# Performance work log

Measured on AMD Instinct MI355X. Metric: run time of the kernel, lower is better.

## Reference

```python
import jax, jax.numpy as jnp
import numpy as np

B, N, D, H = 4, 2048, 1024, 64

def setup_inputs() -> dict:
    key = jax.random.key(0)
    ks = jax.random.split(key, 7)
    s = D ** -0.5  # torch Linear default init scale ~ U(-1/sqrt(fan_in), ...); scale randn similarly
    return {
        "x":  jax.random.normal(ks[0], (B, N, D), dtype=jnp.float32),
        "Wq": jax.random.normal(ks[1], (D, H), dtype=jnp.float32) * s,
        "bq": jax.random.normal(ks[2], (H,), dtype=jnp.float32) * s,
        "Wk": jax.random.normal(ks[3], (D, H), dtype=jnp.float32) * s,
        "bk": jax.random.normal(ks[4], (H,), dtype=jnp.float32) * s,
        "Wv": jax.random.normal(ks[5], (D, H), dtype=jnp.float32) * s,
        "bv": jax.random.normal(ks[6], (H,), dtype=jnp.float32) * s,
    }

def reference(x, Wq, bq, Wk, bk, Wv, bv):
    head_size = Wq.shape[1]
    q = x @ Wq + bq          # [B, N, H]
    k = x @ Wk + bk          # [B, N, H]
    v = x @ Wv + bv          # [B, N, H]
    scores = jnp.einsum("bid,bjd->bij", q, k)        # [B, N, N]
    # faithful to torch: keep upper triangle (col >= row), then mask exact zeros to -inf
    scores = jnp.triu(scores)
    scores = jnp.where(scores == 0, -jnp.inf, scores)
    attn = jax.nn.softmax(scores * (head_size ** -0.5), axis=-1)  # [B, N, N]
    # out = (V^T @ attn)^T  ==  attn^T @ V
    out = jnp.einsum("bji,bjh->bih", attn, v)         # [B, N, H]
    return out
```

## Files before the change

kernel.cpp:

```cpp
#include <hip/hip_runtime.h>
#include <math.h>

constexpr int kN = 2048;
constexpr int kD = 1024;

typedef __attribute__((ext_vector_type(8))) short bf16x8;
typedef __attribute__((ext_vector_type(4))) short bf16x4;
typedef __attribute__((ext_vector_type(4))) float f32x4;

#define MFMA(a, b, c) __builtin_amdgcn_mfma_f32_16x16x32_bf16(a, b, c, 0, 0, 0)

__device__ __forceinline__ short f2bf(float f) {
    unsigned u = __float_as_uint(f);
    u += 0x7fff + ((u >> 16) & 1);
    return (short)(u >> 16);
}

__device__ __forceinline__ void g2l(void* lds, const void* g, int nbytes, int t) {
    int lane = t & 63, w = t >> 6;
    for (int base = w * 1024; base < nbytes; base += 4096) {
        if (base + lane * 16 < nbytes) {
            __builtin_amdgcn_global_load_lds(
                (const __attribute__((address_space(1))) void*)((const char*)g + base + lane * 16),
                (__attribute__((address_space(3))) void*)((char*)lds + base),
                16, 0, 0);
        }
    }
}

__global__ __launch_bounds__(256) void prep_kernel(
        const float* __restrict__ Wq, const float* __restrict__ Wk,
        const float* __restrict__ Wv, const float* __restrict__ bq,
        const float* __restrict__ bk, const float* __restrict__ bv,
        short* __restrict__ Wt, float* __restrict__ bcat)
{
    int tid = blockIdx.x * 256 + threadIdx.x;
    int stride = gridDim.x * 256;
    for (int e = tid; e < 16 * 192 * 72; e += stride) {
        int kc = e / (192 * 72);
        int rem = e - kc * (192 * 72);
        int n = rem / 72, c = rem - n * 72;
        short v = 0;
        if (c < 64) {
            int d = kc * 64 + c;
            float wv = (n < 64) ? Wq[d * 64 + n]
                     : (n < 128) ? Wk[d * 64 + (n - 64)]
                     : Wv[d * 64 + (n - 128)];
            v = f2bf(wv);
        }
        Wt[e] = v;
    }
    if (tid < 192)
        bcat[tid] = (tid < 64) ? bq[tid] : (tid < 128) ? bk[tid - 64] : bv[tid - 128];
}

__global__ __launch_bounds__(256) void qkv_kernel(
        const float* __restrict__ x, const short* __restrict__ Wt,
        const float* __restrict__ bcat,
        short* __restrict__ gq, short* __restrict__ gk, short* __restrict__ vt)
{
    __shared__ __align__(16) short xs[2][16 * 72];
    __shared__ __align__(16) short wsm[2][192 * 72];
    const int t = threadIdx.x;
    const int w = t >> 6, lane = t & 63, l15 = lane & 15, q8 = lane >> 4;
    const int m0 = blockIdx.x * 16;
    const int xrow = t >> 4, xc4 = t & 15;
    const float* xbase = x + (size_t)(m0 + xrow) * kD + xc4 * 4;

    f32x4 acc[3];
    #pragma unroll
    for (int ct = 0; ct < 3; ++ct) acc[ct] = (f32x4){0.f, 0.f, 0.f, 0.f};

    float4 xcur = *(const float4*)(xbase + 0 * 64);
    g2l(wsm[0], Wt, 192 * 144, t);
    {
        bf16x4 pk = {f2bf(xcur.x), f2bf(xcur.y), f2bf(xcur.z), f2bf(xcur.w)};
        *(bf16x4*)&xs[0][xrow * 72 + xc4 * 4] = pk;
    }
    float4 xnxt = *(const float4*)(xbase + 1 * 64);
    __syncthreads();

    for (int kc = 0; kc < 16; ++kc) {
        const int cur = kc & 1, nb = cur ^ 1;
        if (kc < 15)
            g2l(wsm[nb], Wt + (size_t)(kc + 1) * 192 * 72, 192 * 144, t);

        bf16x8 a0 = *(const bf16x8*)&xs[cur][l15 * 72 + q8 * 8];
        bf16x8 a1 = *(const bf16x8*)&xs[cur][l15 * 72 + 32 + q8 * 8];
        #pragma unroll
        for (int ct = 0; ct < 3; ++ct) {
            int brow = w * 48 + ct * 16 + l15;
            bf16x8 b0 = *(const bf16x8*)&wsm[cur][brow * 72 + q8 * 8];
            bf16x8 b1 = *(const bf16x8*)&wsm[cur][brow * 72 + 32 + q8 * 8];
            acc[ct] = MFMA(a0, b0, acc[ct]);
            acc[ct] = MFMA(a1, b1, acc[ct]);
        }
        if (kc < 15) {
            bf16x4 pk = {f2bf(xnxt.x), f2bf(xnxt.y), f2bf(xnxt.z), f2bf(xnxt.w)};
            *(bf16x4*)&xs[nb][xrow * 72 + xc4 * 4] = pk;
            if (kc < 14)
                xnxt = *(const float4*)(xbase + (kc + 2) * 64);
        }
        __syncthreads();
    }

    const int bz = m0 >> 11;
    const int jt = (m0 & 2047) >> 6;
    const int jb = m0 & 63;
    #pragma unroll
    for (int ct = 0; ct < 3; ++ct) {
        int nb2 = w * 48 + ct * 16;
        int n = nb2 + l15;
        float bias = bcat[n];
        if (nb2 < 64) {
            #pragma unroll
            for (int r = 0; r < 4; ++r)
                gq[(size_t)(m0 + q8 * 4 + r) * 72 + n] = f2bf(acc[ct][r] + bias);
        } else if (nb2 < 128) {
            #pragma unroll
            for (int r = 0; r < 4; ++r)
                gk[(size_t)(m0 + q8 * 4 + r) * 72 + (n - 64)] = f2bf(acc[ct][r] + bias);
        } else {
            int h = n - 128;
            bf16x4 pk = {f2bf(acc[ct][0] + bias), f2bf(acc[ct][1] + bias),
                         f2bf(acc[ct][2] + bias), f2bf(acc[ct][3] + bias)};
            *(bf16x4*)&vt[((size_t)((bz * 32 + jt) * 64 + h)) * 72 + jb + q8 * 4] = pk;
        }
    }
}

__global__ __launch_bounds__(256) void stats_kernel(
        const short* __restrict__ gq, const short* __restrict__ gk,
        float* __restrict__ l2)
{
    __shared__ __align__(16) short qsm[64 * 72];
    __shared__ __align__(16) short ksm[2][64 * 72];
    const int t = threadIdx.x;
    const int w = t >> 6, lane = t & 63, l15 = lane & 15, q8 = lane >> 4;
    const int b = blockIdx.x;
    const int ic = b & 3, bz = (b >> 2) & 3, jt = b >> 4;
    const int j0 = jt * 64;
    const int ilo = ic * 512, ihi = ilo + 512;
    const int istart = (j0 > ilo) ? j0 : ilo;
    const int count = (istart < ihi) ? ((ihi - istart) >> 6) : 0;

    float lloc[4] = {0.f, 0.f, 0.f, 0.f};

    if (count > 0) {
        g2l(qsm, gq + (size_t)(bz * kN + j0) * 72, 64 * 144, t);
        g2l(ksm[0], gk + (size_t)(bz * kN + istart) * 72, 64 * 144, t);
        __syncthreads();
        int jrow = 16 * w + l15;
        bf16x8 a0 = *(const bf16x8*)&qsm[jrow * 72 + q8 * 8];
        bf16x8 a1 = *(const bf16x8*)&qsm[jrow * 72 + 32 + q8 * 8];

        for (int idx = 0; idx < count; ++idx) {
            const int cur = idx & 1;
            if (idx + 1 < count)
                g2l(ksm[cur ^ 1],
                    gk + (size_t)(bz * kN + istart + (idx + 1) * 64) * 72, 64 * 144, t);
            const int i0 = istart + idx * 64;
            #pragma unroll
            for (int it = 0; it < 4; ++it) {
                int irow = it * 16 + l15;
                bf16x8 b0 = *(const bf16x8*)&ksm[cur][irow * 72 + q8 * 8];
                bf16x8 b1 = *(const bf16x8*)&ksm[cur][irow * 72 + 32 + q8 * 8];
                f32x4 s = (f32x4){0.f, 0.f, 0.f, 0.f};
                s = MFMA(a0, b0, s);
                s = MFMA(a1, b1, s);
                int ig = i0 + it * 16 + l15;
                #pragma unroll
                for (int r = 0; r < 4; ++r) {
                    int jg = j0 + 16 * w + q8 * 4 + r;
                    float sv = s[r];
                    float e = __expf(sv * 0.125f);
                    lloc[r] += ((ig >= jg) && (sv != 0.0f)) ? e : 0.0f;
                }
            }
            __syncthreads();
        }
    }
    #pragma unroll
    for (int off = 1; off < 16; off <<= 1)
        #pragma unroll
        for (int r = 0; r < 4; ++r)
            lloc[r] += __shfl_xor(lloc[r], off);
    if (l15 == 0) {
        #pragma unroll
        for (int r = 0; r < 4; ++r)
            l2[ic * 8192 + bz * kN + j0 + 16 * w + q8 * 4 + r] = lloc[r];
    }
}

__global__ __launch_bounds__(256) void out_kernel(
        const short* __restrict__ gq, const short* __restrict__ gk,
        const short* __restrict__ vt, const float* __restrict__ l2,
        float* __restrict__ part)
{
    __shared__ __align__(16) short ksm[64 * 72];
    __shared__ __align__(16) short qsm[2][64 * 72];
    __shared__ __align__(16) short vsm[2][64 * 72];
    __shared__ __align__(16) short psm[64 * 72];
    __shared__ float rsm[2][64];
    const int t = threadIdx.x;
    const int w = t >> 6, lane = t & 63, l15 = lane & 15, q8 = lane >> 4;
    const int b = blockIdx.x;
    const int jc = b & 3, bz = (b >> 2) & 3, it = b >> 4;
    const int i0 = it * 64;
    const int jlo = jc * 512;
    const int jhi = (jlo + 512 < i0 + 64) ? (jlo + 512) : (i0 + 64);
    const int count = (jlo < jhi) ? ((jhi - jlo) >> 6) : 0;

    f32x4 oacc[4];
    #pragma unroll
    for (int i = 0; i < 4; ++i) oacc[i] = (f32x4){0.f, 0.f, 0.f, 0.f};

    if (count > 0) {
        g2l(ksm, gk + (size_t)(bz * kN + i0) * 72, 64 * 144, t);
        g2l(qsm[0], gq + (size_t)(bz * kN + jlo) * 72, 64 * 144, t);
        g2l(vsm[0], vt + (size_t)((bz * 32 + (jlo >> 6)) * 64) * 72, 64 * 144, t);
        if (t < 64) {
            int j = bz * kN + jlo + t;
            float l = l2[j] + l2[8192 + j] + l2[16384 + j] + l2[24576 + j];
            rsm[0][t] = (l > 0.f) ? 1.0f / l : 0.0f;
        }
        __syncthreads();

        for (int idx = 0; idx < count; ++idx) {
            const int cur = idx & 1, nb = cur ^ 1;
            const int j0s = jlo + idx * 64;
            if (idx + 1 < count) {
                g2l(qsm[nb], gq + (size_t)(bz * kN + j0s + 64) * 72, 64 * 144, t);
                g2l(vsm[nb], vt + (size_t)((bz * 32 + ((j0s + 64) >> 6)) * 64) * 72,
                    64 * 144, t);
                if (t < 64) {
                    int j = bz * kN + j0s + 64 + t;
                    float l = l2[j] + l2[8192 + j] + l2[16384 + j] + l2[24576 + j];
                    rsm[nb][t] = (l > 0.f) ? 1.0f / l : 0.0f;
                }
            }
            int jrow = 16 * w + l15;
            bf16x8 a0 = *(const bf16x8*)&qsm[cur][jrow * 72 + q8 * 8];
            bf16x8 a1 = *(const bf16x8*)&qsm[cur][jrow * 72 + 32 + q8 * 8];
            #pragma unroll
            for (int itile = 0; itile < 4; ++itile) {
                int irow = itile * 16 + l15;
                bf16x8 b0 = *(const bf16x8*)&ksm[irow * 72 + q8 * 8];
                bf16x8 b1 = *(const bf16x8*)&ksm[irow * 72 + 32 + q8 * 8];
                f32x4 s = (f32x4){0.f, 0.f, 0.f, 0.f};
                s = MFMA(a0, b0, s);
                s = MFMA(a1, b1, s);
                int ig = i0 + itile * 16 + l15;
                bf16x4 pk;
                #pragma unroll
                for (int r = 0; r < 4; ++r) {
                    int jl = 16 * w + q8 * 4 + r;
                    int jg = j0s + jl;
                    float sv = s[r];
                    float p = ((ig >= jg) && (sv != 0.0f))
                            ? __expf(sv * 0.125f) * rsm[cur][jl] : 0.0f;
                    pk[r] = f2bf(p);
                }
                *(bf16x4*)&psm[(itile * 16 + l15) * 72 + 16 * w + q8 * 4] = pk;
            }
            __syncthreads();

            bf16x8 pa0 = *(const bf16x8*)&psm[(16 * w + l15) * 72 + q8 * 8];
            bf16x8 pa1 = *(const bf16x8*)&psm[(16 * w + l15) * 72 + 32 + q8 * 8];
            #pragma unroll
            for (int ht = 0; ht < 4; ++ht) {
                int vrow = ht * 16 + l15;
                bf16x8 vb0 = *(const bf16x8*)&vsm[cur][vrow * 72 + q8 * 8];
                bf16x8 vb1 = *(const bf16x8*)&vsm[cur][vrow * 72 + 32 + q8 * 8];
                oacc[ht] = MFMA(pa0, vb0, oacc[ht]);
                oacc[ht] = MFMA(pa1, vb1, oacc[ht]);
            }
            __syncthreads();
        }
    }
    size_t base = ((size_t)(jc * 4 + bz) * kN + i0) * 64;
    #pragma unroll
    for (int ht = 0; ht < 4; ++ht)
        #pragma unroll
        for (int r = 0; r < 4; ++r)
            part[base + (size_t)(16 * w + q8 * 4 + r) * 64 + ht * 16 + l15] = oacc[ht][r];
}

__global__ __launch_bounds__(256) void reduce_kernel(
        const float* __restrict__ part, float* __restrict__ out)
{
    int idx = blockIdx.x * 256 + threadIdx.x;
    const float4* p = (const float4*)part;
    float4 a = p[idx];
    float4 b = p[idx + 131072];
    float4 c = p[idx + 262144];
    float4 d = p[idx + 393216];
    float4 r;
    r.x = a.x + b.x + c.x + d.x;
    r.y = a.y + b.y + c.y + d.y;
    r.z = a.z + b.z + c.z + d.z;
    r.w = a.w + b.w + c.w + d.w;
    ((float4*)out)[idx] = r;
}

extern "C" void kernel_launch(void* const* d_in, const int* in_sizes, int n_in,
                              void* d_out, int out_size, void* d_ws, size_t ws_size,
                              hipStream_t stream)
{
    const float* x  = (const float*)d_in[0];
    const float* Wq = (const float*)d_in[1];
    const float* bq = (const float*)d_in[2];
    const float* Wk = (const float*)d_in[3];
    const float* bk = (const float*)d_in[4];
    const float* Wv = (const float*)d_in[5];
    const float* bv = (const float*)d_in[6];
    float* out = (float*)d_out;

    char* base = (char*)d_ws;
    short* Wt   = (short*)(base);
    float* bcat = (float*)(base + 442368);
    short* gq   = (short*)(base + 443392);
    short* gk   = (short*)(base + 1623040);
    short* vt   = (short*)(base + 2802688);
    float* l2   = (float*)(base + 3982336);
    float* part = (float*)(base + 4113408);

    prep_kernel<<<128, 256, 0, stream>>>(Wq, Wk, Wv, bq, bk, bv, Wt, bcat);
    qkv_kernel<<<512, 256, 0, stream>>>(x, Wt, bcat, gq, gk, vt);
    stats_kernel<<<512, 256, 0, stream>>>(gq, gk, l2);
    out_kernel<<<512, 256, 0, stream>>>(gq, gk, vt, l2, part);
    reduce_kernel<<<512, 256, 0, stream>>>(part, out);
}
```

Measured before the change: 134.9 us.

## Double QKV row tile and split attention output over two balanced halves

The QKV projection kernel now handles 32 rows per block instead of 16. Each staged weight tile is reused across two MFMA row tiles, which halves the global weight traffic, at the cost of more accumulator registers and half as many blocks. The output kernel no longer cuts the key range into four fixed 512-wide chunks, many of them empty. It now splits each causal row range into two roughly equal halves, so work per block is more even and there are fewer partial sums to write. The reduce kernel now adds only two partials, but the longest output blocks do up to 16 tiles in sequence, which can lengthen the critical path.

```diff
diff --git a/kernel.cpp b/kernel.cpp
--- a/kernel.cpp
+++ b/kernel.cpp
@@ -59,25 +59,32 @@
         const float* __restrict__ bcat,
         short* __restrict__ gq, short* __restrict__ gk, short* __restrict__ vt)
 {
-    __shared__ __align__(16) short xs[2][16 * 72];
+    __shared__ __align__(16) short xs[2][32 * 72];
     __shared__ __align__(16) short wsm[2][192 * 72];
     const int t = threadIdx.x;
     const int w = t >> 6, lane = t & 63, l15 = lane & 15, q8 = lane >> 4;
-    const int m0 = blockIdx.x * 16;
+    const int m0 = blockIdx.x * 32;
     const int xrow = t >> 4, xc4 = t & 15;
-    const float* xbase = x + (size_t)(m0 + xrow) * kD + xc4 * 4;
-
-    f32x4 acc[3];
-    #pragma unroll
-    for (int ct = 0; ct < 3; ++ct) acc[ct] = (f32x4){0.f, 0.f, 0.f, 0.f};
-
-    float4 xcur = *(const float4*)(xbase + 0 * 64);
+    const float* xb0 = x + (size_t)(m0 + xrow) * kD + xc4 * 4;
+    const float* xb1 = xb0 + 16 * kD;
+
+    f32x4 acc[2][3];
+    #pragma unroll
+    for (int rt = 0; rt < 2; ++rt)
+        #pragma unroll
+        for (int ct = 0; ct < 3; ++ct) acc[rt][ct] = (f32x4){0.f, 0.f, 0.f, 0.f};
+
+    float4 xc0 = *(const float4*)(xb0);
+    float4 xc1 = *(const float4*)(xb1);
     g2l(wsm[0], Wt, 192 * 144, t);
     {
-        bf16x4 pk = {f2bf(xcur.x), f2bf(xcur.y), f2bf(xcur.z), f2bf(xcur.w)};
-        *(bf16x4*)&xs[0][xrow * 72 + xc4 * 4] = pk;
-    }
-    float4 xnxt = *(const float4*)(xbase + 1 * 64);
+        bf16x4 p0 = {f2bf(xc0.x), f2bf(xc0.y), f2bf(xc0.z), f2bf(xc0.w)};
+        bf16x4 p1 = {f2bf(xc1.x), f2bf(xc1.y), f2bf(xc1.z), f2bf(xc1.w)};
+        *(bf16x4*)&xs[0][xrow * 72 + xc4 * 4] = p0;
+        *(bf16x4*)&xs[0][(xrow + 16) * 72 + xc4 * 4] = p1;
+    }
+    float4 xn0 = *(const float4*)(xb0 + 64);
+    float4 xn1 = *(const float4*)(xb1 + 64);
     __syncthreads();
 
     for (int kc = 0; kc < 16; ++kc) {
@@ -85,21 +92,35 @@
         if (kc < 15)
             g2l(wsm[nb], Wt + (size_t)(kc + 1) * 192 * 72, 192 * 144, t);
 
-        bf16x8 a0 = *(const bf16x8*)&xs[cur][l15 * 72 + q8 * 8];
-        bf16x8 a1 = *(const bf16x8*)&xs[cur][l15 * 72 + 32 + q8 * 8];
+        bf16x8 a[2][2], b[3][2];
+        #pragma unroll
+        for (int rt = 0; rt < 2; ++rt) {
+            int arow = rt * 16 + l15;
+            a[rt][0] = *(const bf16x8*)&xs[cur][arow * 72 + q8 * 8];
+            a[rt][1] = *(const bf16x8*)&xs[cur][arow * 72 + 32 + q8 * 8];
+        }
         #pragma unroll
         for (int ct = 0; ct < 3; ++ct) {
             int brow = w * 48 + ct * 16 + l15;
-            bf16x8 b0 = *(const bf16x8*)&wsm[cur][brow * 72 + q8 * 8];
-            bf16x8 b1 = *(const bf16x8*)&wsm[cur][brow * 72 + 32 + q8 * 8];
-            acc[ct] = MFMA(a0, b0, acc[ct]);
-            acc[ct] = MFMA(a1, b1, acc[ct]);
-        }
+            b[ct][0] = *(const bf16x8*)&wsm[cur][brow * 72 + q8 * 8];
+            b[ct][1] = *(const bf16x8*)&wsm[cur][brow * 72 + 32 + q8 * 8];
+        }
+        #pragma unroll
+        for (int rt = 0; rt < 2; ++rt)
+            #pragma unroll
+            for (int ct = 0; ct < 3; ++ct) {
+                acc[rt][ct] = MFMA(a[rt][0], b[ct][0], acc[rt][ct]);
+                acc[rt][ct] = MFMA(a[rt][1], b[ct][1], acc[rt][ct]);
+            }
         if (kc < 15) {
-            bf16x4 pk = {f2bf(xnxt.x), f2bf(xnxt.y), f2bf(xnxt.z), f2bf(xnxt.w)};
-            *(bf16x4*)&xs[nb][xrow * 72 + xc4 * 4] = pk;
-            if (kc < 14)
-                xnxt = *(const float4*)(xbase + (kc + 2) * 64);
+            bf16x4 p0 = {f2bf(xn0.x), f2bf(xn0.y), f2bf(xn0.z), f2bf(xn0.w)};
+            bf16x4 p1 = {f2bf(xn1.x), f2bf(xn1.y), f2bf(xn1.z), f2bf(xn1.w)};
+            *(bf16x4*)&xs[nb][xrow * 72 + xc4 * 4] = p0;
+            *(bf16x4*)&xs[nb][(xrow + 16) * 72 + xc4 * 4] = p1;
+            if (kc < 14) {
+                xn0 = *(const float4*)(xb0 + (kc + 2) * 64);
+                xn1 = *(const float4*)(xb1 + (kc + 2) * 64);
+            }
         }
         __syncthreads();
     }
@@ -108,25 +129,30 @@
     const int jt = (m0 & 2047) >> 6;
     const int jb = m0 & 63;
     #pragma unroll
-    for (int ct = 0; ct < 3; ++ct) {
-        int nb2 = w * 48 + ct * 16;
-        int n = nb2 + l15;
-        float bias = bcat[n];
-        if (nb2 < 64) {
-            #pragma unroll
-            for (int r = 0; r < 4; ++r)
-                gq[(size_t)(m0 + q8 * 4 + r) * 72 + n] = f2bf(acc[ct][r] + bias);
-        } else if (nb2 < 128) {
-            #pragma unroll
-            for (int r = 0; r < 4; ++r)
-                gk[(size_t)(m0 + q8 * 4 + r) * 72 + (n - 64)] = f2bf(acc[ct][r] + bias);
-        } else {
-            int h = n - 128;
-            bf16x4 pk = {f2bf(acc[ct][0] + bias), f2bf(acc[ct][1] + bias),
-                         f2bf(acc[ct][2] + bias), f2bf(acc[ct][3] + bias)};
-            *(bf16x4*)&vt[((size_t)((bz * 32 + jt) * 64 + h)) * 72 + jb + q8 * 4] = pk;
-        }
-    }
+    for (int rt = 0; rt < 2; ++rt)
+        #pragma unroll
+        for (int ct = 0; ct < 3; ++ct) {
+            int nb2 = w * 48 + ct * 16;
+            int n = nb2 + l15;
+            float bias = bcat[n];
+            if (nb2 < 64) {
+                #pragma unroll
+                for (int r = 0; r < 4; ++r)
+                    gq[(size_t)(m0 + rt * 16 + q8 * 4 + r) * 72 + n] =
+                        f2bf(acc[rt][ct][r] + bias);
+            } else if (nb2 < 128) {
+                #pragma unroll
+                for (int r = 0; r < 4; ++r)
+                    gk[(size_t)(m0 + rt * 16 + q8 * 4 + r) * 72 + (n - 64)] =
+                        f2bf(acc[rt][ct][r] + bias);
+            } else {
+                int h = n - 128;
+                bf16x4 pk = {f2bf(acc[rt][ct][0] + bias), f2bf(acc[rt][ct][1] + bias),
+                             f2bf(acc[rt][ct][2] + bias), f2bf(acc[rt][ct][3] + bias)};
+                *(bf16x4*)&vt[((size_t)((bz * 32 + jt) * 64 + h)) * 72
+                              + jb + rt * 16 + q8 * 4] = pk;
+            }
+        }
 }
 
 __global__ __launch_bounds__(256) void stats_kernel(
@@ -205,11 +231,11 @@
     const int t = threadIdx.x;
     const int w = t >> 6, lane = t & 63, l15 = lane & 15, q8 = lane >> 4;
     const int b = blockIdx.x;
-    const int jc = b & 3, bz = (b >> 2) & 3, it = b >> 4;
+    const int s = b & 1, bz = (b >> 1) & 3, it = b >> 3;
     const int i0 = it * 64;
-    const int jlo = jc * 512;
-    const int jhi = (jlo + 512 < i0 + 64) ? (jlo + 512) : (i0 + 64);
-    const int count = (jlo < jhi) ? ((jhi - jlo) >> 6) : 0;
+    const int h0 = (it + 2) >> 1;
+    const int count = s == 0 ? h0 : (it + 1 - h0);
+    const int jlo = s == 0 ? 0 : h0 * 64;
 
     f32x4 oacc[4];
     #pragma unroll
@@ -247,16 +273,16 @@
                 int irow = itile * 16 + l15;
                 bf16x8 b0 = *(const bf16x8*)&ksm[irow * 72 + q8 * 8];
                 bf16x8 b1 = *(const bf16x8*)&ksm[irow * 72 + 32 + q8 * 8];
-                f32x4 s = (f32x4){0.f, 0.f, 0.f, 0.f};
-                s = MFMA(a0, b0, s);
-                s = MFMA(a1, b1, s);
+                f32x4 sv4 = (f32x4){0.f, 0.f, 0.f, 0.f};
+                sv4 = MFMA(a0, b0, sv4);
+                sv4 = MFMA(a1, b1, sv4);
                 int ig = i0 + itile * 16 + l15;
                 bf16x4 pk;
                 #pragma unroll
                 for (int r = 0; r < 4; ++r) {
                     int jl = 16 * w + q8 * 4 + r;
                     int jg = j0s + jl;
-                    float sv = s[r];
+                    float sv = sv4[r];
                     float p = ((ig >= jg) && (sv != 0.0f))
                             ? __expf(sv * 0.125f) * rsm[cur][jl] : 0.0f;
                     pk[r] = f2bf(p);
@@ -278,7 +304,7 @@
             __syncthreads();
         }
     }
-    size_t base = ((size_t)(jc * 4 + bz) * kN + i0) * 64;
+    size_t base = ((size_t)(s * 4 + bz) * kN + i0) * 64;
     #pragma unroll
     for (int ht = 0; ht < 4; ++ht)
         #pragma unroll
@@ -293,13 +319,11 @@
     const float4* p = (const float4*)part;
     float4 a = p[idx];
     float4 b = p[idx + 131072];
-    float4 c = p[idx + 262144];
-    float4 d = p[idx + 393216];
     float4 r;
-    r.x = a.x + b.x + c.x + d.x;
-    r.y = a.y + b.y + c.y + d.y;
-    r.z = a.z + b.z + c.z + d.z;
-    r.w = a.w + b.w + c.w + d.w;
+    r.x = a.x + b.x;
+    r.y = a.y + b.y;
+    r.z = a.z + b.z;
+    r.w = a.w + b.w;
     ((float4*)out)[idx] = r;
 }
 
@@ -326,8 +350,8 @@
     float* part = (float*)(base + 4113408);
 
     prep_kernel<<<128, 256, 0, stream>>>(Wq, Wk, Wv, bq, bk, bv, Wt, bcat);
-    qkv_kernel<<<512, 256, 0, stream>>>(x, Wt, bcat, gq, gk, vt);
+    qkv_kernel<<<256, 256, 0, stream>>>(x, Wt, bcat, gq, gk, vt);
     stats_kernel<<<512, 256, 0, stream>>>(gq, gk, l2);
-    out_kernel<<<512, 256, 0, stream>>>(gq, gk, vt, l2, part);
+    out_kernel<<<256, 256, 0, stream>>>(gq, gk, vt, l2, part);
     reduce_kernel<<<512, 256, 0, stream>>>(part, out);
 }
```

Measured after the change: 151.8 us. 12.6% more time.

## Fuse five kernel launches into one cooperative persistent kernel with grid syncs

Applied to the files above, without the earlier changes.

Merges the prep, QKV projection, stats, output and reduce kernels into a single cooperative kernel of 512 blocks that separates the phases with grid-wide barriers and shares one LDS buffer. The goal is to remove the launch overhead and inter-kernel gaps between the five stages. If the cooperative launch fails, it falls back to the original separate launches. The cost is grid-sync latency and phases that are each limited to a fixed 512-block grid. Occupancy may also change, since the 60 KB shared buffer is now requested for every phase.

```diff
diff --git a/kernel.cpp b/kernel.cpp
--- a/kernel.cpp
+++ b/kernel.cpp
@@ -1,8 +1,12 @@
 #include <hip/hip_runtime.h>
+#include <hip/hip_cooperative_groups.h>
 #include <math.h>
+
+namespace cg = cooperative_groups;
 
 constexpr int kN = 2048;
 constexpr int kD = 1024;
+constexpr int SMEM_BYTES = 60416;
 
 typedef __attribute__((ext_vector_type(8))) short bf16x8;
 typedef __attribute__((ext_vector_type(4))) short bf16x4;
@@ -28,15 +32,15 @@
     }
 }
 
-__global__ __launch_bounds__(256) void prep_kernel(
+
+__device__ __forceinline__ void phase_prep(int blk, int t,
         const float* __restrict__ Wq, const float* __restrict__ Wk,
         const float* __restrict__ Wv, const float* __restrict__ bq,
         const float* __restrict__ bk, const float* __restrict__ bv,
         short* __restrict__ Wt, float* __restrict__ bcat)
 {
-    int tid = blockIdx.x * 256 + threadIdx.x;
-    int stride = gridDim.x * 256;
-    for (int e = tid; e < 16 * 192 * 72; e += stride) {
+    int tid = blk * 256 + t;
+    for (int e = tid; e < 16 * 192 * 72; e += 512 * 256) {
         int kc = e / (192 * 72);
         int rem = e - kc * (192 * 72);
         int n = rem / 72, c = rem - n * 72;
@@ -54,16 +58,15 @@
         bcat[tid] = (tid < 64) ? bq[tid] : (tid < 128) ? bk[tid - 64] : bv[tid - 128];
 }
 
-__global__ __launch_bounds__(256) void qkv_kernel(
+__device__ __forceinline__ void phase_qkv(int blk, int t, char* smem,
         const float* __restrict__ x, const short* __restrict__ Wt,
         const float* __restrict__ bcat,
         short* __restrict__ gq, short* __restrict__ gk, short* __restrict__ vt)
 {
-    __shared__ __align__(16) short xs[2][16 * 72];
-    __shared__ __align__(16) short wsm[2][192 * 72];
-    const int t = threadIdx.x;
+    short* wsm = (short*)smem;
+    short* xs  = (short*)(smem + 55296);
     const int w = t >> 6, lane = t & 63, l15 = lane & 15, q8 = lane >> 4;
-    const int m0 = blockIdx.x * 16;
+    const int m0 = blk * 16;
     const int xrow = t >> 4, xc4 = t & 15;
     const float* xbase = x + (size_t)(m0 + xrow) * kD + xc4 * 4;
 
@@ -71,33 +74,33 @@
     #pragma unroll
     for (int ct = 0; ct < 3; ++ct) acc[ct] = (f32x4){0.f, 0.f, 0.f, 0.f};
 
-    float4 xcur = *(const float4*)(xbase + 0 * 64);
-    g2l(wsm[0], Wt, 192 * 144, t);
+    float4 xcur = *(const float4*)(xbase);
+    g2l(wsm, Wt, 192 * 144, t);
     {
         bf16x4 pk = {f2bf(xcur.x), f2bf(xcur.y), f2bf(xcur.z), f2bf(xcur.w)};
-        *(bf16x4*)&xs[0][xrow * 72 + xc4 * 4] = pk;
-    }
-    float4 xnxt = *(const float4*)(xbase + 1 * 64);
+        *(bf16x4*)&xs[xrow * 72 + xc4 * 4] = pk;
+    }
+    float4 xnxt = *(const float4*)(xbase + 64);
     __syncthreads();
 
     for (int kc = 0; kc < 16; ++kc) {
         const int cur = kc & 1, nb = cur ^ 1;
         if (kc < 15)
-            g2l(wsm[nb], Wt + (size_t)(kc + 1) * 192 * 72, 192 * 144, t);
-
-        bf16x8 a0 = *(const bf16x8*)&xs[cur][l15 * 72 + q8 * 8];
-        bf16x8 a1 = *(const bf16x8*)&xs[cur][l15 * 72 + 32 + q8 * 8];
+            g2l(wsm + nb * 13824, Wt + (size_t)(kc + 1) * 192 * 72, 192 * 144, t);
+
+        bf16x8 a0 = *(const bf16x8*)&xs[cur * 1152 + l15 * 72 + q8 * 8];
+        bf16x8 a1 = *(const bf16x8*)&xs[cur * 1152 + l15 * 72 + 32 + q8 * 8];
         #pragma unroll
         for (int ct = 0; ct < 3; ++ct) {
             int brow = w * 48 + ct * 16 + l15;
-            bf16x8 b0 = *(const bf16x8*)&wsm[cur][brow * 72 + q8 * 8];
-            bf16x8 b1 = *(const bf16x8*)&wsm[cur][brow * 72 + 32 + q8 * 8];
+            bf16x8 b0 = *(const bf16x8*)&wsm[cur * 13824 + brow * 72 + q8 * 8];
+            bf16x8 b1 = *(const bf16x8*)&wsm[cur * 13824 + brow * 72 + 32 + q8 * 8];
             acc[ct] = MFMA(a0, b0, acc[ct]);
             acc[ct] = MFMA(a1, b1, acc[ct]);
         }
         if (kc < 15) {
             bf16x4 pk = {f2bf(xnxt.x), f2bf(xnxt.y), f2bf(xnxt.z), f2bf(xnxt.w)};
-            *(bf16x4*)&xs[nb][xrow * 72 + xc4 * 4] = pk;
+            *(bf16x4*)&xs[nb * 1152 + xrow * 72 + xc4 * 4] = pk;
             if (kc < 14)
                 xnxt = *(const float4*)(xbase + (kc + 2) * 64);
         }
@@ -129,16 +132,14 @@
     }
 }
 
-__global__ __launch_bounds__(256) void stats_kernel(
+__device__ __forceinline__ void phase_stats(int blk, int t, char* smem,
         const short* __restrict__ gq, const short* __restrict__ gk,
         float* __restrict__ l2)
 {
-    __shared__ __align__(16) short qsm[64 * 72];
-    __shared__ __align__(16) short ksm[2][64 * 72];
-    const int t = threadIdx.x;
+    short* qsm = (short*)smem;
+    short* ksm = (short*)(smem + 9216);
     const int w = t >> 6, lane = t & 63, l15 = lane & 15, q8 = lane >> 4;
-    const int b = blockIdx.x;
-    const int ic = b & 3, bz = (b >> 2) & 3, jt = b >> 4;
+    const int ic = blk & 3, bz = (blk >> 2) & 3, jt = blk >> 4;
     const int j0 = jt * 64;
     const int ilo = ic * 512, ihi = ilo + 512;
     const int istart = (j0 > ilo) ? j0 : ilo;
@@ -148,7 +149,7 @@
 
     if (count > 0) {
         g2l(qsm, gq + (size_t)(bz * kN + j0) * 72, 64 * 144, t);
-        g2l(ksm[0], gk + (size_t)(bz * kN + istart) * 72, 64 * 144, t);
+        g2l(ksm, gk + (size_t)(bz * kN + istart) * 72, 64 * 144, t);
         __syncthreads();
         int jrow = 16 * w + l15;
         bf16x8 a0 = *(const bf16x8*)&qsm[jrow * 72 + q8 * 8];
@@ -157,14 +158,14 @@
         for (int idx = 0; idx < count; ++idx) {
             const int cur = idx & 1;
             if (idx + 1 < count)
-                g2l(ksm[cur ^ 1],
+                g2l(ksm + (cur ^ 1) * 4608,
                     gk + (size_t)(bz * kN + istart + (idx + 1) * 64) * 72, 64 * 144, t);
             const int i0 = istart + idx * 64;
             #pragma unroll
             for (int it = 0; it < 4; ++it) {
                 int irow = it * 16 + l15;
-                bf16x8 b0 = *(const bf16x8*)&ksm[cur][irow * 72 + q8 * 8];
-                bf16x8 b1 = *(const bf16x8*)&ksm[cur][irow * 72 + 32 + q8 * 8];
+                bf16x8 b0 = *(const bf16x8*)&ksm[cur * 4608 + irow * 72 + q8 * 8];
+                bf16x8 b1 = *(const bf16x8*)&ksm[cur * 4608 + irow * 72 + 32 + q8 * 8];
                 f32x4 s = (f32x4){0.f, 0.f, 0.f, 0.f};
                 s = MFMA(a0, b0, s);
                 s = MFMA(a1, b1, s);
@@ -192,20 +193,18 @@
     }
 }
 
-__global__ __launch_bounds__(256) void out_kernel(
+__device__ __forceinline__ void phase_out(int blk, int t, char* smem,
         const short* __restrict__ gq, const short* __restrict__ gk,
         const short* __restrict__ vt, const float* __restrict__ l2,
         float* __restrict__ part)
 {
-    __shared__ __align__(16) short ksm[64 * 72];
-    __shared__ __align__(16) short qsm[2][64 * 72];
-    __shared__ __align__(16) short vsm[2][64 * 72];
-    __shared__ __align__(16) short psm[64 * 72];
-    __shared__ float rsm[2][64];
-    const int t = threadIdx.x;
+    short* ksm = (short*)smem;
+    short* qsm = (short*)(smem + 9216);
+    short* vsm = (short*)(smem + 27648);
+    short* psm = (short*)(smem + 46080);
+    float* rsm = (float*)(smem + 55296);
     const int w = t >> 6, lane = t & 63, l15 = lane & 15, q8 = lane >> 4;
-    const int b = blockIdx.x;
-    const int jc = b & 3, bz = (b >> 2) & 3, it = b >> 4;
+    const int jc = blk & 3, bz = (blk >> 2) & 3, it = blk >> 4;
     const int i0 = it * 64;
     const int jlo = jc * 512;
     const int jhi = (jlo + 512 < i0 + 64) ? (jlo + 512) : (i0 + 64);
@@ -217,12 +216,12 @@
 
     if (count > 0) {
         g2l(ksm, gk + (size_t)(bz * kN + i0) * 72, 64 * 144, t);
-        g2l(qsm[0], gq + (size_t)(bz * kN + jlo) * 72, 64 * 144, t);
-        g2l(vsm[0], vt + (size_t)((bz * 32 + (jlo >> 6)) * 64) * 72, 64 * 144, t);
+        g2l(qsm, gq + (size_t)(bz * kN + jlo) * 72, 64 * 144, t);
+        g2l(vsm, vt + (size_t)((bz * 32 + (jlo >> 6)) * 64) * 72, 64 * 144, t);
         if (t < 64) {
             int j = bz * kN + jlo + t;
             float l = l2[j] + l2[8192 + j] + l2[16384 + j] + l2[24576 + j];
-            rsm[0][t] = (l > 0.f) ? 1.0f / l : 0.0f;
+            rsm[t] = (l > 0.f) ? 1.0f / l : 0.0f;
         }
         __syncthreads();
 
@@ -230,35 +229,35 @@
             const int cur = idx & 1, nb = cur ^ 1;
             const int j0s = jlo + idx * 64;
             if (idx + 1 < count) {
-                g2l(qsm[nb], gq + (size_t)(bz * kN + j0s + 64) * 72, 64 * 144, t);
-                g2l(vsm[nb], vt + (size_t)((bz * 32 + ((j0s + 64) >> 6)) * 64) * 72,
-                    64 * 144, t);
+                g2l(qsm + nb * 4608, gq + (size_t)(bz * kN + j0s + 64) * 72, 64 * 144, t);
+                g2l(vsm + nb * 4608,
+                    vt + (size_t)((bz * 32 + ((j0s + 64) >> 6)) * 64) * 72, 64 * 144, t);
                 if (t < 64) {
                     int j = bz * kN + j0s + 64 + t;
                     float l = l2[j] + l2[8192 + j] + l2[16384 + j] + l2[24576 + j];
-                    rsm[nb][t] = (l > 0.f) ? 1.0f / l : 0.0f;
+                    rsm[nb * 64 + t] = (l > 0.f) ? 1.0f / l : 0.0f;
                 }
             }
             int jrow = 16 * w + l15;
-            bf16x8 a0 = *(const bf16x8*)&qsm[cur][jrow * 72 + q8 * 8];
-            bf16x8 a1 = *(const bf16x8*)&qsm[cur][jrow * 72 + 32 + q8 * 8];
+            bf16x8 a0 = *(const bf16x8*)&qsm[cur * 4608 + jrow * 72 + q8 * 8];
+            bf16x8 a1 = *(const bf16x8*)&qsm[cur * 4608 + jrow * 72 + 32 + q8 * 8];
             #pragma unroll
             for (int itile = 0; itile < 4; ++itile) {
                 int irow = itile * 16 + l15;
                 bf16x8 b0 = *(const bf16x8*)&ksm[irow * 72 + q8 * 8];
                 bf16x8 b1 = *(const bf16x8*)&ksm[irow * 72 + 32 + q8 * 8];
-                f32x4 s = (f32x4){0.f, 0.f, 0.f, 0.f};
-                s = MFMA(a0, b0, s);
-                s = MFMA(a1, b1, s);
+                f32x4 sv4 = (f32x4){0.f, 0.f, 0.f, 0.f};
+                sv4 = MFMA(a0, b0, sv4);
+                sv4 = MFMA(a1, b1, sv4);
                 int ig = i0 + itile * 16 + l15;
                 bf16x4 pk;
                 #pragma unroll
                 for (int r = 0; r < 4; ++r) {
                     int jl = 16 * w + q8 * 4 + r;
                     int jg = j0s + jl;
-                    float sv = s[r];
+                    float sv = sv4[r];
                     float p = ((ig >= jg) && (sv != 0.0f))
-                            ? __expf(sv * 0.125f) * rsm[cur][jl] : 0.0f;
+                            ? __expf(sv * 0.125f) * rsm[cur * 64 + jl] : 0.0f;
                     pk[r] = f2bf(p);
                 }
                 *(bf16x4*)&psm[(itile * 16 + l15) * 72 + 16 * w + q8 * 4] = pk;
@@ -270,8 +269,8 @@
             #pragma unroll
             for (int ht = 0; ht < 4; ++ht) {
                 int vrow = ht * 16 + l15;
-                bf16x8 vb0 = *(const bf16x8*)&vsm[cur][vrow * 72 + q8 * 8];
-                bf16x8 vb1 = *(const bf16x8*)&vsm[cur][vrow * 72 + 32 + q8 * 8];
+                bf16x8 vb0 = *(const bf16x8*)&vsm[cur * 4608 + vrow * 72 + q8 * 8];
+                bf16x8 vb1 = *(const bf16x8*)&vsm[cur * 4608 + vrow * 72 + 32 + q8 * 8];
                 oacc[ht] = MFMA(pa0, vb0, oacc[ht]);
                 oacc[ht] = MFMA(pa1, vb1, oacc[ht]);
             }
@@ -286,10 +285,10 @@
             part[base + (size_t)(16 * w + q8 * 4 + r) * 64 + ht * 16 + l15] = oacc[ht][r];
 }
 
-__global__ __launch_bounds__(256) void reduce_kernel(
+__device__ __forceinline__ void phase_reduce(int blk, int t,
         const float* __restrict__ part, float* __restrict__ out)
 {
-    int idx = blockIdx.x * 256 + threadIdx.x;
+    int idx = blk * 256 + t;
     const float4* p = (const float4*)part;
     float4 a = p[idx];
     float4 b = p[idx + 131072];
@@ -303,6 +302,67 @@
     ((float4*)out)[idx] = r;
 }
 
+__global__ __launch_bounds__(256, 2) void fused_kernel(
+        const float* x, const float* Wq, const float* bq, const float* Wk,
+        const float* bk, const float* Wv, const float* bv, float* out,
+        short* Wt, float* bcat, short* gq, short* gk, short* vt,
+        float* l2, float* part)
+{
+    __shared__ __align__(16) char smem[SMEM_BYTES];
+    cg::grid_group grid = cg::this_grid();
+    const int blk = blockIdx.x, t = threadIdx.x;
+    phase_prep(blk, t, Wq, Wk, Wv, bq, bk, bv, Wt, bcat);
+    grid.sync();
+    phase_qkv(blk, t, smem, x, Wt, bcat, gq, gk, vt);
+    grid.sync();
+    phase_stats(blk, t, smem, gq, gk, l2);
+    grid.sync();
+    phase_out(blk, t, smem, gq, gk, vt, l2, part);
+    grid.sync();
+    phase_reduce(blk, t, part, out);
+}
+
+__global__ __launch_bounds__(256) void prep_kernel(
+        const float* __restrict__ Wq, const float* __restrict__ Wk,
+        const float* __restrict__ Wv, const float* __restrict__ bq,
+        const float* __restrict__ bk, const float* __restrict__ bv,
+        short* __restrict__ Wt, float* __restrict__ bcat)
+{
+    phase_prep(blockIdx.x, threadIdx.x, Wq, Wk, Wv, bq, bk, bv, Wt, bcat);
+}
+
+__global__ __launch_bounds__(256) void qkv_kernel(
+        const float* __restrict__ x, const short* __restrict__ Wt,
+        const float* __restrict__ bcat,
+        short* __restrict__ gq, short* __restrict__ gk, short* __restrict__ vt)
+{
+    __shared__ __align__(16) char smem[SMEM_BYTES];
+    phase_qkv(blockIdx.x, threadIdx.x, smem, x, Wt, bcat, gq, gk, vt);
+}
+
+__global__ __launch_bounds__(256) void stats_kernel(
+        const short* __restrict__ gq, const short* __restrict__ gk,
+        float* __restrict__ l2)
+{
+    __shared__ __align__(16) char smem[SMEM_BYTES];
+    phase_stats(blockIdx.x, threadIdx.x, smem, gq, gk, l2);
+}
+
+__global__ __launch_bounds__(256) void out_kernel(
+        const short* __restrict__ gq, const short* __restrict__ gk,
+        const short* __restrict__ vt, const float* __restrict__ l2,
+        float* __restrict__ part)
+{
+    __shared__ __align__(16) char smem[SMEM_BYTES];
+    phase_out(blockIdx.x, threadIdx.x, smem, gq, gk, vt, l2, part);
+}
+
+__global__ __launch_bounds__(256) void reduce_kernel(
+        const float* __restrict__ part, float* __restrict__ out)
+{
+    phase_reduce(blockIdx.x, threadIdx.x, part, out);
+}
+
 extern "C" void kernel_launch(void* const* d_in, const int* in_sizes, int n_in,
                               void* d_out, int out_size, void* d_ws, size_t ws_size,
                               hipStream_t stream)
@@ -325,9 +385,19 @@
     float* l2   = (float*)(base + 3982336);
     float* part = (float*)(base + 4113408);
 
-    prep_kernel<<<128, 256, 0, stream>>>(Wq, Wk, Wv, bq, bk, bv, Wt, bcat);
-    qkv_kernel<<<512, 256, 0, stream>>>(x, Wt, bcat, gq, gk, vt);
-    stats_kernel<<<512, 256, 0, stream>>>(gq, gk, l2);
-    out_kernel<<<512, 256, 0, stream>>>(gq, gk, vt, l2, part);
-    reduce_kernel<<<512, 256, 0, stream>>>(part, out);
-}
+    void* args[] = {
+        (void*)&x, (void*)&Wq, (void*)&bq, (void*)&Wk, (void*)&bk,
+        (void*)&Wv, (void*)&bv, (void*)&out, (void*)&Wt, (void*)&bcat,
+        (void*)&gq, (void*)&gk, (void*)&vt, (void*)&l2, (void*)&part
+    };
+    hipError_t err = hipLaunchCooperativeKernel(
+        (void*)fused_kernel, dim3(512), dim3(256), args, 0, stream);
+
+    if (err != hipSuccess) {
+        prep_kernel<<<512, 256, 0, stream>>>(Wq, Wk, Wv, bq, bk, bv, Wt, bcat);
+        qkv_kernel<<<512, 256, 0, stream>>>(x, Wt, bcat, gq, gk, vt);
+        stats_kernel<<<512, 256, 0, stream>>>(gq, gk, l2);
+        out_kernel<<<512, 256, 0, stream>>>(gq, gk, vt, l2, part);
+        reduce_kernel<<<512, 256, 0, stream>>>(part, out);
+    }
+}
```

Measured after the change: 364.3 us. +170.1%, slower.

## Pre-swizzle weights into MFMA fragment order and fold softmax normalizer into V

Applied to the files above, without the earlier changes.

The weight prep now writes bf16 weights directly in per-lane MFMA fragment order, so the QKV kernel reads B operands straight from global/L2 instead of staging them through double-buffered LDS with a barrier each step. The block instead converts its full 16x1024 x tile into LDS up front. A new vscale kernel multiplies V rows by the reciprocal row-sum once, which removes the per-tile l2 loads and multiplies from out_kernel. This adds a kernel launch and an extra bf16 rounding of scaled V, and relies on cache hits for the uncoalesced-per-wave weight reads.

```diff
diff --git a/kernel.cpp b/kernel.cpp
--- a/kernel.cpp
+++ b/kernel.cpp
@@ -14,6 +14,9 @@
     unsigned u = __float_as_uint(f);
     u += 0x7fff + ((u >> 16) & 1);
     return (short)(u >> 16);
+}
+__device__ __forceinline__ float bf2f(short s) {
+    return __uint_as_float(((unsigned)(unsigned short)s) << 16);
 }
 
 __device__ __forceinline__ void g2l(void* lds, const void* g, int nbytes, int t) {
@@ -36,72 +39,68 @@
 {
     int tid = blockIdx.x * 256 + threadIdx.x;
     int stride = gridDim.x * 256;
-    for (int e = tid; e < 16 * 192 * 72; e += stride) {
-        int kc = e / (192 * 72);
-        int rem = e - kc * (192 * 72);
-        int n = rem / 72, c = rem - n * 72;
-        short v = 0;
-        if (c < 64) {
-            int d = kc * 64 + c;
-            float wv = (n < 64) ? Wq[d * 64 + n]
-                     : (n < 128) ? Wk[d * 64 + (n - 64)]
-                     : Wv[d * 64 + (n - 128)];
-            v = f2bf(wv);
-        }
-        Wt[e] = v;
+    for (int e = tid; e < 16 * 12 * 2 * 512; e += stride) {
+        int kc = e / 12288;
+        int rem = e - kc * 12288;
+        int nt = rem >> 10;
+        int r2 = rem & 1023;
+        int f = r2 >> 9;
+        int r3 = r2 & 511;
+        int q8 = r3 >> 7;
+        int l15 = (r3 >> 3) & 15;
+        int el = r3 & 7;
+        int n = nt * 16 + l15;
+        int d = kc * 64 + f * 32 + q8 * 8 + el;
+        float wv = (n < 64) ? Wq[d * 64 + n]
+                 : (n < 128) ? Wk[d * 64 + (n - 64)]
+                 : Wv[d * 64 + (n - 128)];
+        Wt[e] = f2bf(wv);
     }
     if (tid < 192)
         bcat[tid] = (tid < 64) ? bq[tid] : (tid < 128) ? bk[tid - 64] : bv[tid - 128];
 }
+
+constexpr int XP = 1032;
 
 __global__ __launch_bounds__(256) void qkv_kernel(
         const float* __restrict__ x, const short* __restrict__ Wt,
         const float* __restrict__ bcat,
         short* __restrict__ gq, short* __restrict__ gk, short* __restrict__ vt)
 {
-    __shared__ __align__(16) short xs[2][16 * 72];
-    __shared__ __align__(16) short wsm[2][192 * 72];
+    __shared__ __align__(16) short xs[16 * XP];
     const int t = threadIdx.x;
     const int w = t >> 6, lane = t & 63, l15 = lane & 15, q8 = lane >> 4;
     const int m0 = blockIdx.x * 16;
-    const int xrow = t >> 4, xc4 = t & 15;
-    const float* xbase = x + (size_t)(m0 + xrow) * kD + xc4 * 4;
+
+    {
+        int row = t >> 4, c4 = (t & 15) * 4;
+        const float* xr = x + (size_t)(m0 + row) * kD;
+        #pragma unroll
+        for (int cc = 0; cc < 16; ++cc) {
+            float4 xv = *(const float4*)&xr[cc * 64 + c4];
+            bf16x4 pk = {f2bf(xv.x), f2bf(xv.y), f2bf(xv.z), f2bf(xv.w)};
+            *(bf16x4*)&xs[row * XP + cc * 64 + c4] = pk;
+        }
+    }
+    __syncthreads();
 
     f32x4 acc[3];
     #pragma unroll
     for (int ct = 0; ct < 3; ++ct) acc[ct] = (f32x4){0.f, 0.f, 0.f, 0.f};
 
-    float4 xcur = *(const float4*)(xbase + 0 * 64);
-    g2l(wsm[0], Wt, 192 * 144, t);
-    {
-        bf16x4 pk = {f2bf(xcur.x), f2bf(xcur.y), f2bf(xcur.z), f2bf(xcur.w)};
-        *(bf16x4*)&xs[0][xrow * 72 + xc4 * 4] = pk;
-    }
-    float4 xnxt = *(const float4*)(xbase + 1 * 64);
-    __syncthreads();
-
+    #pragma unroll 4
     for (int kc = 0; kc < 16; ++kc) {
-        const int cur = kc & 1, nb = cur ^ 1;
-        if (kc < 15)
-            g2l(wsm[nb], Wt + (size_t)(kc + 1) * 192 * 72, 192 * 144, t);
-
-        bf16x8 a0 = *(const bf16x8*)&xs[cur][l15 * 72 + q8 * 8];
-        bf16x8 a1 = *(const bf16x8*)&xs[cur][l15 * 72 + 32 + q8 * 8];
+        bf16x8 a0 = *(const bf16x8*)&xs[l15 * XP + kc * 64 + q8 * 8];
+        bf16x8 a1 = *(const bf16x8*)&xs[l15 * XP + kc * 64 + 32 + q8 * 8];
         #pragma unroll
         for (int ct = 0; ct < 3; ++ct) {
-            int brow = w * 48 + ct * 16 + l15;
-            bf16x8 b0 = *(const bf16x8*)&wsm[cur][brow * 72 + q8 * 8];
-            bf16x8 b1 = *(const bf16x8*)&wsm[cur][brow * 72 + 32 + q8 * 8];
+            int nt = w * 3 + ct;
+            const short* bp = Wt + ((size_t)(kc * 12 + nt) * 2) * 512 + lane * 8;
+            bf16x8 b0 = *(const bf16x8*)bp;
+            bf16x8 b1 = *(const bf16x8*)(bp + 512);
             acc[ct] = MFMA(a0, b0, acc[ct]);
             acc[ct] = MFMA(a1, b1, acc[ct]);
         }
-        if (kc < 15) {
-            bf16x4 pk = {f2bf(xnxt.x), f2bf(xnxt.y), f2bf(xnxt.z), f2bf(xnxt.w)};
-            *(bf16x4*)&xs[nb][xrow * 72 + xc4 * 4] = pk;
-            if (kc < 14)
-                xnxt = *(const float4*)(xbase + (kc + 2) * 64);
-        }
-        __syncthreads();
     }
 
     const int bz = m0 >> 11;
@@ -192,16 +191,38 @@
     }
 }
 
+__global__ __launch_bounds__(256) void vscale_kernel(
+        short* __restrict__ vt, const float* __restrict__ l2)
+{
+    __shared__ float rsm[64];
+    const int g = blockIdx.x, t = threadIdx.x;
+    if (t < 64) {
+        int j = (g >> 5) * kN + (g & 31) * 64 + t;
+        float l = l2[j] + l2[8192 + j] + l2[16384 + j] + l2[24576 + j];
+        rsm[t] = (l > 0.f) ? 1.0f / l : 0.0f;
+    }
+    __syncthreads();
+    const int h = t >> 2, c0 = (t & 3) * 16;
+    size_t base = ((size_t)g * 64 + h) * 72 + c0;
+    #pragma unroll
+    for (int bb = 0; bb < 2; ++bb) {
+        bf16x8 v = *(bf16x8*)&vt[base + bb * 8];
+        bf16x8 o;
+        #pragma unroll
+        for (int e = 0; e < 8; ++e)
+            o[e] = f2bf(bf2f(v[e]) * rsm[c0 + bb * 8 + e]);
+        *(bf16x8*)&vt[base + bb * 8] = o;
+    }
+}
+
 __global__ __launch_bounds__(256) void out_kernel(
         const short* __restrict__ gq, const short* __restrict__ gk,
-        const short* __restrict__ vt, const float* __restrict__ l2,
-        float* __restrict__ part)
+        const short* __restrict__ vt, float* __restrict__ part)
 {
     __shared__ __align__(16) short ksm[64 * 72];
     __shared__ __align__(16) short qsm[2][64 * 72];
     __shared__ __align__(16) short vsm[2][64 * 72];
     __shared__ __align__(16) short psm[64 * 72];
-    __shared__ float rsm[2][64];
     const int t = threadIdx.x;
     const int w = t >> 6, lane = t & 63, l15 = lane & 15, q8 = lane >> 4;
     const int b = blockIdx.x;
@@ -219,11 +240,6 @@
         g2l(ksm, gk + (size_t)(bz * kN + i0) * 72, 64 * 144, t);
         g2l(qsm[0], gq + (size_t)(bz * kN + jlo) * 72, 64 * 144, t);
         g2l(vsm[0], vt + (size_t)((bz * 32 + (jlo >> 6)) * 64) * 72, 64 * 144, t);
-        if (t < 64) {
-            int j = bz * kN + jlo + t;
-            float l = l2[j] + l2[8192 + j] + l2[16384 + j] + l2[24576 + j];
-            rsm[0][t] = (l > 0.f) ? 1.0f / l : 0.0f;
-        }
         __syncthreads();
 
         for (int idx = 0; idx < count; ++idx) {
@@ -233,11 +249,6 @@
                 g2l(qsm[nb], gq + (size_t)(bz * kN + j0s + 64) * 72, 64 * 144, t);
                 g2l(vsm[nb], vt + (size_t)((bz * 32 + ((j0s + 64) >> 6)) * 64) * 72,
                     64 * 144, t);
-                if (t < 64) {
-                    int j = bz * kN + j0s + 64 + t;
-                    float l = l2[j] + l2[8192 + j] + l2[16384 + j] + l2[24576 + j];
-                    rsm[nb][t] = (l > 0.f) ? 1.0f / l : 0.0f;
-                }
             }
             int jrow = 16 * w + l15;
             bf16x8 a0 = *(const bf16x8*)&qsm[cur][jrow * 72 + q8 * 8];
@@ -247,18 +258,16 @@
                 int irow = itile * 16 + l15;
                 bf16x8 b0 = *(const bf16x8*)&ksm[irow * 72 + q8 * 8];
                 bf16x8 b1 = *(const bf16x8*)&ksm[irow * 72 + 32 + q8 * 8];
-                f32x4 s = (f32x4){0.f, 0.f, 0.f, 0.f};
-                s = MFMA(a0, b0, s);
-                s = MFMA(a1, b1, s);
+                f32x4 sv4 = (f32x4){0.f, 0.f, 0.f, 0.f};
+                sv4 = MFMA(a0, b0, sv4);
+                sv4 = MFMA(a1, b1, sv4);
                 int ig = i0 + itile * 16 + l15;
                 bf16x4 pk;
                 #pragma unroll
                 for (int r = 0; r < 4; ++r) {
-                    int jl = 16 * w + q8 * 4 + r;
-                    int jg = j0s + jl;
-                    float sv = s[r];
-                    float p = ((ig >= jg) && (sv != 0.0f))
-                            ? __expf(sv * 0.125f) * rsm[cur][jl] : 0.0f;
+                    int jg = j0s + 16 * w + q8 * 4 + r;
+                    float sv = sv4[r];
+                    float p = ((ig >= jg) && (sv != 0.0f)) ? __expf(sv * 0.125f) : 0.0f;
                     pk[r] = f2bf(p);
                 }
                 *(bf16x4*)&psm[(itile * 16 + l15) * 72 + 16 * w + q8 * 4] = pk;
@@ -318,16 +327,17 @@
 
     char* base = (char*)d_ws;
     short* Wt   = (short*)(base);
-    float* bcat = (float*)(base + 442368);
-    short* gq   = (short*)(base + 443392);
-    short* gk   = (short*)(base + 1623040);
-    short* vt   = (short*)(base + 2802688);
-    float* l2   = (float*)(base + 3982336);
-    float* part = (float*)(base + 4113408);
-
-    prep_kernel<<<128, 256, 0, stream>>>(Wq, Wk, Wv, bq, bk, bv, Wt, bcat);
+    float* bcat = (float*)(base + 393216);
+    short* gq   = (short*)(base + 394240);
+    short* gk   = (short*)(base + 1573888);
+    short* vt   = (short*)(base + 2753536);
+    float* l2   = (float*)(base + 3933184);
+    float* part = (float*)(base + 4064256);
+
+    prep_kernel<<<256, 256, 0, stream>>>(Wq, Wk, Wv, bq, bk, bv, Wt, bcat);
     qkv_kernel<<<512, 256, 0, stream>>>(x, Wt, bcat, gq, gk, vt);
     stats_kernel<<<512, 256, 0, stream>>>(gq, gk, l2);
-    out_kernel<<<512, 256, 0, stream>>>(gq, gk, vt, l2, part);
+    vscale_kernel<<<128, 256, 0, stream>>>(vt, l2);
+    out_kernel<<<512, 256, 0, stream>>>(gq, gk, vt, part);
     reduce_kernel<<<512, 256, 0, stream>>>(part, out);
 }
```

Measured after the change: 126.3 us, median of 2. -6.3%, faster.
